# Kernel optimization log

Hardware: AMD Instinct MI355X
Metric: run time of the kernel (lower is better)

## Reference

```python
import jax, jax.numpy as jnp
import numpy as np

N_ROI = 116; G = 128; DEG = 32
N = G * N_ROI          # 14848 nodes
E = G * N_ROI * DEG    # 475136 edges
HID = 64; HEADS = 4; HC = HEADS * HID  # 256
EDIM = 5; EMB = 16; NG = 8; OUT = 2
NEG = 0.01      # nn.LeakyReLU default slope
NEG_ATT = 0.2   # GATv2 internal negative_slope
EPS = 1e-5


def leaky(x, s=NEG):
    return jnp.where(x >= 0, x, s * x)


def seg_softmax(logits, seg, n):
    # numerically stable softmax over edges grouped by target node
    m = jax.ops.segment_max(logits, seg, num_segments=n)
    m = jnp.where(jnp.isfinite(m), m, 0.0)
    ex = jnp.exp(logits - m[seg])
    s = jax.ops.segment_sum(ex, seg, num_segments=n)
    return ex / (s[seg] + 1e-16)


def _xav(k, shape):
    return jax.random.normal(k, shape, jnp.float32) * np.sqrt(2.0 / sum(shape)).astype(np.float32)


def setup_inputs() -> dict:
    key = jax.random.key(0)
    ks = jax.random.split(key, 40)
    x = jax.random.normal(ks[0], (N, N_ROI), jnp.float32)
    off = (jnp.arange(G, dtype=jnp.int32) * N_ROI)[:, None]
    src = (jax.random.randint(ks[1], (G, N_ROI * DEG), 0, N_ROI, jnp.int32) + off).reshape(-1)
    dst = (jax.random.randint(ks[2], (G, N_ROI * DEG), 0, N_ROI, jnp.int32) + off).reshape(-1)
    edge_index = jnp.stack([src, dst])  # [2, E], block-diagonal per graph
    edge_attr = jax.random.normal(ks[3], (E, EDIM), jnp.float32)
    grp = np.repeat(np.arange(NG, dtype=np.int32), [15] * 7 + [11])  # partition of 116 ROIs
    node_group = jnp.tile(jnp.asarray(grp), G)
    batch = jnp.repeat(jnp.arange(G, dtype=jnp.int32), N_ROI)
    p = {
        'group_emb': _xav(ks[4], (NG, EMB)),
        'W_embed': _xav(ks[5], (N_ROI + EMB, HID)), 'b_embed': jnp.zeros((HID,), jnp.float32),
        'We_enc': _xav(ks[6], (EDIM, HID)), 'be_enc': jnp.zeros((HID,), jnp.float32),
        'W1': _xav(ks[7], (HID, HID)), 'b1': jnp.zeros((HID,), jnp.float32),
        'W2': _xav(ks[8], (HID, HID)), 'b2': jnp.zeros((HID,), jnp.float32),
        'ln_g': jnp.ones((HID,), jnp.float32), 'ln_b': jnp.zeros((HID,), jnp.float32),
        'l0_Wl': _xav(ks[9], (HID, HC)), 'l0_Wr': _xav(ks[10], (HID, HC)),
        'l0_We': _xav(ks[11], (EDIM, HC)), 'l0_att': _xav(ks[12], (HEADS, HID)),
        'l0_b': jnp.zeros((HC,), jnp.float32),
        'l0_bn_g': jnp.ones((HC,), jnp.float32), 'l0_bn_b': jnp.zeros((HC,), jnp.float32),
        'l1_Wl': _xav(ks[13], (HC, HC)), 'l1_Wr': _xav(ks[14], (HC, HC)),
        'l1_We': _xav(ks[15], (EDIM, HC)), 'l1_att': _xav(ks[16], (HEADS, HID)),
        'l1_b': jnp.zeros((HC,), jnp.float32),
        'l1_bn_g': jnp.ones((HC,), jnp.float32), 'l1_bn_b': jnp.zeros((HC,), jnp.float32),
        'fc2_W': _xav(ks[17], (HC, OUT)), 'fc2_b': jnp.zeros((OUT,), jnp.float32),
    }
    return dict(x=x, edge_index=edge_index, edge_attr=edge_attr, batch=batch, node_group=node_group, **p)


def _gat_layer(h, src, dst, edge_attr, Wl, Wr, We, att, b, bn_g, bn_b):
    n = h.shape[0]
    xl = (h @ Wl).reshape(n, HEADS, HID)
    xr = (h @ Wr).reshape(n, HEADS, HID)
    e = (edge_attr @ We).reshape(-1, HEADS, HID)
    xls = xl[src]                                   # [E,H,C]
    z = leaky(xls + xr[dst] + e, NEG_ATT)
    logits = jnp.einsum('ehc,hc->eh', z, att)       # GATv2 attention scores
    alpha = seg_softmax(logits, dst, n)             # softmax over incoming edges per node
    out = jax.ops.segment_sum(xls * alpha[:, :, None], dst, num_segments=n)
    out = out.reshape(n, HC) + b
    mu = out.mean(0); var = ((out - mu) ** 2).mean(0)  # BatchNorm (batch stats)
    out = (out - mu) / jnp.sqrt(var + EPS) * bn_g + bn_b
    return leaky(out)


def reference(x, edge_index, edge_attr, batch, node_group, group_emb, W_embed, b_embed,
              We_enc, be_enc, W1, b1, W2, b2, ln_g, ln_b,
              l0_Wl, l0_Wr, l0_We, l0_att, l0_b, l0_bn_g, l0_bn_b,
              l1_Wl, l1_Wr, l1_We, l1_att, l1_b, l1_bn_g, l1_bn_b, fc2_W, fc2_b):
    src, dst = edge_index[0], edge_index[1]
    # BrainEncodeEmbed: group embedding concat + projection
    h = jnp.concatenate([x, group_emb[node_group]], axis=-1)   # [N, 132]
    h = leaky(h @ W_embed + b_embed)                            # [N, HID]
    eemb = leaky(edge_attr @ We_enc + be_enc)                   # [E, HID]
    # GINEConv: sum_j ReLU(x_j + e_ij), eps=0, then MLP
    msg = jax.nn.relu(h[src] + eemb)
    h = h + jax.ops.segment_sum(msg, dst, num_segments=N)
    h = leaky(h @ W1 + b1) @ W2 + b2
    h = leaky(h)
    mu = h.mean(-1, keepdims=True)
    v = ((h - mu) ** 2).mean(-1, keepdims=True)
    h = (h - mu) / jnp.sqrt(v + EPS) * ln_g + ln_b              # LayerNorm
    # stacked GATv2 blocks
    h = _gat_layer(h, src, dst, edge_attr, l0_Wl, l0_Wr, l0_We, l0_att, l0_b, l0_bn_g, l0_bn_b)
    h = _gat_layer(h, src, dst, edge_attr, l1_Wl, l1_Wr, l1_We, l1_att, l1_b, l1_bn_g, l1_bn_b)
    # global mean pool + classifier
    cnt = jax.ops.segment_sum(jnp.ones((h.shape[0],), h.dtype), batch, num_segments=G)
    pooled = jax.ops.segment_sum(h, batch, num_segments=G) / cnt[:, None]
    return pooled @ fc2_W + fc2_b
```

## Files before the change

### kernel.cpp

```cpp
#include <hip/hip_runtime.h>
#include <hip/hip_bf16.h>

#define NN     14848
#define NE     475136
#define NROI   116
#define NGRAPH 128
#define EPG    3712
#define HID    64
#define HC     256
#define NEG    0.01f
#define NEGA   0.2f
#define EPB    2304
#define XPAD   65

typedef __attribute__((ext_vector_type(8))) short short8;
typedef __attribute__((ext_vector_type(4))) float floatx4;

__device__ __forceinline__ float leaky(float x, float s) { return fmaxf(x, s * x); }

__device__ __forceinline__ short f2bf(float f) {
    unsigned u = __float_as_uint(f);
    unsigned r = (u + 0x7fffu + ((u >> 16) & 1u)) >> 16;
    return (short)r;
}

__global__ __launch_bounds__(256) void k_embed(
    const float* __restrict__ x, const int* __restrict__ ng,
    const float* __restrict__ gemb, const float* __restrict__ W,
    const float* __restrict__ b, float* __restrict__ h0)
{
    const int w = threadIdx.x >> 6, c = threadIdx.x & 63;
    const int n = blockIdx.x * 4 + w;
    __shared__ float in[4][132];
    for (int k = c; k < NROI; k += 64) in[w][k] = x[n * NROI + k];
    if (c < 16) in[w][NROI + c] = gemb[ng[n] * 16 + c];
    __syncthreads();
    float acc = b[c];
    #pragma unroll 4
    for (int k = 0; k < 132; k++) acc = fmaf(in[w][k], W[k * 64 + c], acc);
    h0[n * 64 + c] = leaky(acc, NEG);
}

__global__ __launch_bounds__(256) void k_csr(
    const int* __restrict__ src, const int* __restrict__ dst,
    const float* __restrict__ ea,
    int* __restrict__ row_start, int* __restrict__ row_cnt,
    int* __restrict__ ssd, float* __restrict__ ea_s,
    float* __restrict__ stats01)
{
    const int g = blockIdx.x, tid = threadIdx.x;
    if (g < 2) {
        for (int i = tid; i < 512; i += 256) stats01[g * 512 + i] = 0.f;
    }
    const int e0 = g * EPG, nb = g * NROI;
    __shared__ int cnt[NROI], start[NROI], cur[NROI];
    if (tid < NROI) cnt[tid] = 0;
    __syncthreads();
    for (int i = tid; i < EPG; i += 256) atomicAdd(&cnt[dst[e0 + i] - nb], 1);
    __syncthreads();
    if (tid == 0) {
        int s = 0;
        for (int r = 0; r < NROI; r++) { start[r] = s; s += cnt[r]; }
    }
    __syncthreads();
    if (tid < NROI) {
        row_start[nb + tid] = e0 + start[tid];
        row_cnt[nb + tid] = cnt[tid];
        cur[tid] = start[tid];
    }
    __syncthreads();
    for (int i = tid; i < EPG; i += 256) {
        const int e = e0 + i, dl = dst[e] - nb;
        const int pos = atomicAdd(&cur[dl], 1);
        const int gi = e0 + pos;
        ssd[gi] = (src[e] - nb) | (dl << 16);
        const float4 q = make_float4(ea[e * 5], ea[e * 5 + 1], ea[e * 5 + 2], ea[e * 5 + 3]);
        *(float4*)&ea_s[(size_t)gi * 8] = q;
        ea_s[(size_t)gi * 8 + 4] = ea[e * 5 + 4];
    }
}

__global__ __launch_bounds__(64) void k_prep_w(
    const float* __restrict__ Wl0, const float* __restrict__ Wr0,
    const float* __restrict__ Wl1, const float* __restrict__ Wr1,
    short* __restrict__ Wt0, short* __restrict__ Wt1)
{
    if (blockIdx.x < 512) {
        const int n = blockIdx.x;
        for (int k = threadIdx.x; k < 64; k += 64) {
            const float v = (n < 256) ? Wl0[k * 256 + n] : Wr0[k * 256 + (n - 256)];
            Wt0[(size_t)n * 64 + k] = f2bf(v);
        }
    } else {
        const int n = blockIdx.x - 512;
        for (int k = threadIdx.x; k < 256; k += 64) {
            const float v = (n < 256) ? Wl1[k * 256 + n] : Wr1[k * 256 + (n - 256)];
            Wt1[(size_t)n * 256 + k] = f2bf(v);
        }
    }
}

__global__ __launch_bounds__(256) void k_gine_mlp_ln(
    const float* __restrict__ h0, const int* __restrict__ row_start,
    const int* __restrict__ row_cnt, const int* __restrict__ ssd,
    const float* __restrict__ ea_s,
    const float* __restrict__ We, const float* __restrict__ be,
    const float* __restrict__ W1, const float* __restrict__ b1,
    const float* __restrict__ W2, const float* __restrict__ b2,
    const float* __restrict__ lg_, const float* __restrict__ lb_,
    short* __restrict__ hn)
{
    const int tid = threadIdx.x, w = tid >> 6, lane = tid & 63;
    const int row = blockIdx.x * 4 + w;
    const int nb = (row / NROI) * NROI;
    const int st = row_start[row], cnt = row_cnt[row];
    const float w0 = We[lane], w1 = We[64 + lane], w2 = We[128 + lane],
                w3 = We[192 + lane], w4 = We[256 + lane];
    const float bec = be[lane];
    float g0 = 0.f, g1 = 0.f;
    int j = 0;
    for (; j + 2 <= cnt; j += 2) {
        const int ia = st + j, ib = st + j + 1;
        const int sa = nb + (ssd[ia] & 0xffff), sb = nb + (ssd[ib] & 0xffff);
        const float4 qa = *(const float4*)&ea_s[(size_t)ia * 8];
        const float qa4 = ea_s[(size_t)ia * 8 + 4];
        const float4 qb = *(const float4*)&ea_s[(size_t)ib * 8];
        const float qb4 = ea_s[(size_t)ib * 8 + 4];
        float ea_ = bec, eb_ = bec;
        ea_ = fmaf(qa.x, w0, ea_); eb_ = fmaf(qb.x, w0, eb_);
        ea_ = fmaf(qa.y, w1, ea_); eb_ = fmaf(qb.y, w1, eb_);
        ea_ = fmaf(qa.z, w2, ea_); eb_ = fmaf(qb.z, w2, eb_);
        ea_ = fmaf(qa.w, w3, ea_); eb_ = fmaf(qb.w, w3, eb_);
        ea_ = fmaf(qa4, w4, ea_);  eb_ = fmaf(qb4, w4, eb_);
        g0 += fmaxf(h0[sa * 64 + lane] + leaky(ea_, NEG), 0.f);
        g1 += fmaxf(h0[sb * 64 + lane] + leaky(eb_, NEG), 0.f);
    }
    for (; j < cnt; j++) {
        const int idx = st + j;
        const int s = nb + (ssd[idx] & 0xffff);
        const float4 q = *(const float4*)&ea_s[(size_t)idx * 8];
        const float q4 = ea_s[(size_t)idx * 8 + 4];
        float em = bec;
        em = fmaf(q.x, w0, em); em = fmaf(q.y, w1, em); em = fmaf(q.z, w2, em);
        em = fmaf(q.w, w3, em); em = fmaf(q4, w4, em);
        g0 += fmaxf(h0[s * 64 + lane] + leaky(em, NEG), 0.f);
    }
    const float aggv = g0 + g1;
    __shared__ float v[4][64], t[4][64];
    v[w][lane] = h0[row * 64 + lane] + aggv;
    __syncthreads();
    float a = b1[lane];
    #pragma unroll 8
    for (int k = 0; k < 64; k++) a = fmaf(v[w][k], W1[k * 64 + lane], a);
    t[w][lane] = leaky(a, NEG);
    __syncthreads();
    float o = b2[lane];
    #pragma unroll 8
    for (int k = 0; k < 64; k++) o = fmaf(t[w][k], W2[k * 64 + lane], o);
    o = leaky(o, NEG);
    float s = o;
    #pragma unroll
    for (int off = 32; off; off >>= 1) s += __shfl_xor(s, off);
    const float mu = s * (1.f / 64.f);
    const float d = o - mu;
    float s2 = d * d;
    #pragma unroll
    for (int off = 32; off; off >>= 1) s2 += __shfl_xor(s2, off);
    hn[row * 64 + lane] = f2bf(d * rsqrtf(s2 * (1.f / 64.f) + 1e-5f) * lg_[lane] + lb_[lane]);
}

template <int D, bool BN>
__global__ __launch_bounds__(256) void k_gemm(
    const short* __restrict__ A, const float* __restrict__ Vin,
    const float* __restrict__ stats, const float* __restrict__ bn_g,
    const float* __restrict__ bn_b,
    const short* __restrict__ Wt,
    float* __restrict__ X, float* __restrict__ Y)
{
    const int m0 = blockIdx.x * 16;
    const int w = threadIdx.x >> 6, lane = threadIdx.x & 63;
    const int n0 = w * 128;
    const int r = lane & 15, q = lane >> 4;
    __shared__ float sc_s[256], sh_s[256];
    if constexpr (BN) {
        const int c = threadIdx.x;
        const float inv_n = 1.f / (float)NN;
        const float mu = stats[c] * inv_n;
        float var = stats[256 + c] * inv_n - mu * mu;
        var = fmaxf(var, 0.f);
        const float rsg = rsqrtf(var + 1e-5f) * bn_g[c];
        sc_s[c] = rsg;
        sh_s[c] = bn_b[c] - mu * rsg;
        __syncthreads();
    }
    floatx4 acc[8];
    #pragma unroll
    for (int t = 0; t < 8; t++) acc[t] = (floatx4){0.f, 0.f, 0.f, 0.f};
    const short* Arow = A + (size_t)(m0 + r) * D + q * 8;
    const float* Vrow = Vin + (size_t)(m0 + r) * D + q * 8;
    const short* Brow = Wt + (size_t)(n0 + r) * D + q * 8;
    #pragma unroll
    for (int k0 = 0; k0 < D; k0 += 32) {
        short8 a;
        if constexpr (BN) {
            const float4 v0 = *(const float4*)(Vrow + k0);
            const float4 v1 = *(const float4*)(Vrow + k0 + 4);
            const int cb = q * 8 + k0;
            a[0] = f2bf(leaky(fmaf(v0.x, sc_s[cb + 0], sh_s[cb + 0]), NEG));
            a[1] = f2bf(leaky(fmaf(v0.y, sc_s[cb + 1], sh_s[cb + 1]), NEG));
            a[2] = f2bf(leaky(fmaf(v0.z, sc_s[cb + 2], sh_s[cb + 2]), NEG));
            a[3] = f2bf(leaky(fmaf(v0.w, sc_s[cb + 3], sh_s[cb + 3]), NEG));
            a[4] = f2bf(leaky(fmaf(v1.x, sc_s[cb + 4], sh_s[cb + 4]), NEG));
            a[5] = f2bf(leaky(fmaf(v1.y, sc_s[cb + 5], sh_s[cb + 5]), NEG));
            a[6] = f2bf(leaky(fmaf(v1.z, sc_s[cb + 6], sh_s[cb + 6]), NEG));
            a[7] = f2bf(leaky(fmaf(v1.w, sc_s[cb + 7], sh_s[cb + 7]), NEG));
        } else {
            a = *(const short8*)(Arow + k0);
        }
        #pragma unroll
        for (int t = 0; t < 8; t++) {
            const short8 b = *(const short8*)(Brow + (size_t)t * 16 * D + k0);
            acc[t] = __builtin_amdgcn_mfma_f32_16x16x32_bf16(a, b, acc[t], 0, 0, 0);
        }
    }
    #pragma unroll
    for (int t = 0; t < 8; t++) {
        const int ncol = n0 + t * 16 + r;
        #pragma unroll
        for (int g2 = 0; g2 < 4; g2++) {
            const int row = m0 + q * 4 + g2;
            if (ncol < 256) X[(size_t)row * HC + ncol] = acc[t][g2];
            else            Y[(size_t)row * HC + (ncol - 256)] = acc[t][g2];
        }
    }
}

__global__ __launch_bounds__(256, 4) void k_gat(
    const int* __restrict__ row_start, const int* __restrict__ row_cnt,
    const int* __restrict__ ssd, const float* __restrict__ ea_s,
    const float* __restrict__ We, const float* __restrict__ att,
    const float* __restrict__ bias,
    const float* __restrict__ X, const float* __restrict__ Y,
    float* __restrict__ V, float* __restrict__ stats)
{
    const int g = blockIdx.x >> 3;
    const int h = (blockIdx.x >> 1) & 3;
    const int half = blockIdx.x & 1;
    const int tid = threadIdx.x, w = tid >> 6, lane = tid & 63;
    const int nb = g * NROI, e0 = g * EPG, hc = h * 64;
    const int r0 = half * 58, r1 = r0 + 58;
    const int es = row_start[nb + r0];
    const int ee = (r1 < NROI) ? row_start[nb + r1] : e0 + EPG;

    __shared__ float Xs[NROI * XPAD];
    __shared__ float lg[EPB];
    __shared__ float inv_s[58];

    for (int r = w; r < NROI; r += 4)
        Xs[r * XPAD + lane] = X[(size_t)(nb + r) * HC + hc + lane];
    __syncthreads();

    const int ne = ee - es;
    for (int i = tid; i < ne; i += 256) {
        const int e = es + i;
        const int sd = ssd[e];
        const int sl = sd & 0xffff, dl = sd >> 16;
        const float4 q = *(const float4*)&ea_s[(size_t)e * 8];
        const float q4 = ea_s[(size_t)e * 8 + 4];
        const float* yrow = &Y[(size_t)(nb + dl) * HC + hc];
        const int xb = sl * XPAD;
        float l0 = 0.f, l1 = 0.f;
        #pragma unroll 8
        for (int c = 0; c < 64; c += 2) {
            const float2 y2 = *(const float2*)(yrow + c);
            const float xs0 = Xs[xb + c], xs1 = Xs[xb + c + 1];
            float ep0 = q.x * We[0 * HC + hc + c];
            ep0 = fmaf(q.y, We[1 * HC + hc + c], ep0);
            ep0 = fmaf(q.z, We[2 * HC + hc + c], ep0);
            ep0 = fmaf(q.w, We[3 * HC + hc + c], ep0);
            ep0 = fmaf(q4, We[4 * HC + hc + c], ep0);
            float ep1 = q.x * We[0 * HC + hc + c + 1];
            ep1 = fmaf(q.y, We[1 * HC + hc + c + 1], ep1);
            ep1 = fmaf(q.z, We[2 * HC + hc + c + 1], ep1);
            ep1 = fmaf(q.w, We[3 * HC + hc + c + 1], ep1);
            ep1 = fmaf(q4, We[4 * HC + hc + c + 1], ep1);
            const float z0 = xs0 + y2.x + ep0;
            const float z1 = xs1 + y2.y + ep1;
            l0 = fmaf(att[hc + c], leaky(z0, NEGA), l0);
            l1 = fmaf(att[hc + c + 1], leaky(z1, NEGA), l1);
        }
        lg[i] = l0 + l1;
    }
    __syncthreads();

    for (int r = r0 + w; r < r1; r += 4) {
        const int stl = row_start[nb + r] - es;
        const int cnt = row_cnt[nb + r];
        float m = -INFINITY;
        for (int j = lane; j < cnt; j += 64) m = fmaxf(m, lg[stl + j]);
        #pragma unroll
        for (int off = 32; off; off >>= 1) m = fmaxf(m, __shfl_xor(m, off));
        float s = 0.f;
        for (int j = lane; j < cnt; j += 64) {
            const float e_ = __expf(lg[stl + j] - m);
            lg[stl + j] = e_;
            s += e_;
        }
        #pragma unroll
        for (int off = 32; off; off >>= 1) s += __shfl_xor(s, off);
        if (lane == 0) inv_s[r - r0] = 1.f / (s + 1e-16f);
    }
    __syncthreads();

    float ps = 0.f, ps2 = 0.f;
    const float bb = bias[hc + lane];
    for (int r = r0 + w; r < r1; r += 4) {
        const int st = row_start[nb + r];
        const int cnt = row_cnt[nb + r];
        const int stl = st - es;
        float a0 = 0.f, a1 = 0.f, a2 = 0.f, a3 = 0.f;
        int j = 0;
        for (; j + 4 <= cnt; j += 4) {
            const int s0 = ssd[st + j] & 0xffff, s1 = ssd[st + j + 1] & 0xffff,
                      s2 = ssd[st + j + 2] & 0xffff, s3 = ssd[st + j + 3] & 0xffff;
            a0 = fmaf(Xs[s0 * XPAD + lane], lg[stl + j], a0);
            a1 = fmaf(Xs[s1 * XPAD + lane], lg[stl + j + 1], a1);
            a2 = fmaf(Xs[s2 * XPAD + lane], lg[stl + j + 2], a2);
            a3 = fmaf(Xs[s3 * XPAD + lane], lg[stl + j + 3], a3);
        }
        for (; j < cnt; j++)
            a0 = fmaf(Xs[(ssd[st + j] & 0xffff) * XPAD + lane], lg[stl + j], a0);
        const float vv = ((a0 + a1) + (a2 + a3)) * inv_s[r - r0] + bb;
        V[(size_t)(nb + r) * HC + hc + lane] = vv;
        ps += vv;
        ps2 += vv * vv;
    }
    __syncthreads();
    lg[tid] = ps;
    lg[256 + tid] = ps2;
    __syncthreads();
    if (tid < 64) {
        float s1 = 0.f, s2 = 0.f;
        #pragma unroll
        for (int w2 = 0; w2 < 4; w2++) {
            s1 += lg[w2 * 64 + tid];
            s2 += lg[256 + w2 * 64 + tid];
        }
        atomicAdd(&stats[hc + tid], s1);
        atomicAdd(&stats[256 + hc + tid], s2);
    }
}

__global__ __launch_bounds__(256) void k_pool_fc(
    const float* __restrict__ V, const float* __restrict__ stats,
    const float* __restrict__ bg, const float* __restrict__ bb,
    const float* __restrict__ fW, const float* __restrict__ fb,
    float* __restrict__ out)
{
    const int g = blockIdx.x, c = threadIdx.x;
    const float inv_n = 1.f / (float)NN;
    const float mu = stats[c] * inv_n;
    float var = stats[256 + c] * inv_n - mu * mu;
    var = fmaxf(var, 0.f);
    const float rsg = rsqrtf(var + 1e-5f) * bg[c];
    const float bbc = bb[c];
    float s = 0.f;
    for (int r = 0; r < NROI; r++) {
        const float vv = (V[(size_t)(g * NROI + r) * HC + c] - mu) * rsg + bbc;
        s += leaky(vv, NEG);
    }
    s *= (1.f / (float)NROI);
    __shared__ float red[256];
    for (int o = 0; o < 2; o++) {
        red[c] = s * fW[c * 2 + o];
        __syncthreads();
        for (int off = 128; off; off >>= 1) {
            if (c < off) red[c] += red[c + off];
            __syncthreads();
        }
        if (c == 0) out[g * 2 + o] = red[0] + fb[o];
        __syncthreads();
    }
}

extern "C" void kernel_launch(void* const* d_in, const int* in_sizes, int n_in,
                              void* d_out, int out_size, void* d_ws, size_t ws_size,
                              hipStream_t stream) {
    const float* x         = (const float*)d_in[0];
    const int*   edge_idx  = (const int*)d_in[1];
    const float* edge_attr = (const float*)d_in[2];
    const int*   node_grp  = (const int*)d_in[4];
    const float* group_emb = (const float*)d_in[5];
    const float* W_embed   = (const float*)d_in[6];
    const float* b_embed   = (const float*)d_in[7];
    const float* We_enc    = (const float*)d_in[8];
    const float* be_enc    = (const float*)d_in[9];
    const float* W1        = (const float*)d_in[10];
    const float* b1        = (const float*)d_in[11];
    const float* W2        = (const float*)d_in[12];
    const float* b2        = (const float*)d_in[13];
    const float* ln_g      = (const float*)d_in[14];
    const float* ln_b      = (const float*)d_in[15];
    const float* l0_Wl     = (const float*)d_in[16];
    const float* l0_Wr     = (const float*)d_in[17];
    const float* l0_We     = (const float*)d_in[18];
    const float* l0_att    = (const float*)d_in[19];
    const float* l0_b      = (const float*)d_in[20];
    const float* l0_bn_g   = (const float*)d_in[21];
    const float* l0_bn_b   = (const float*)d_in[22];
    const float* l1_Wl     = (const float*)d_in[23];
    const float* l1_Wr     = (const float*)d_in[24];
    const float* l1_We     = (const float*)d_in[25];
    const float* l1_att    = (const float*)d_in[26];
    const float* l1_b      = (const float*)d_in[27];
    const float* l1_bn_g   = (const float*)d_in[28];
    const float* l1_bn_b   = (const float*)d_in[29];
    const float* fc2_W     = (const float*)d_in[30];
    const float* fc2_b     = (const float*)d_in[31];

    const int* src = edge_idx;
    const int* dst = edge_idx + NE;

    float* ws     = (float*)d_ws;
    float* h0     = ws;
    float* X      = h0 + (size_t)64 * NN;
    float* Y      = X + (size_t)HC * NN;
    float* V      = Y + (size_t)HC * NN;
    float* stats0 = V + (size_t)HC * NN;
    float* stats1 = stats0 + 512;
    float* ea_s   = stats1 + 512;
    int* row_start = (int*)(ea_s + (size_t)8 * NE);
    int* row_cnt   = row_start + NN;
    int* ssd       = row_cnt + NN;
    short* hn_b    = (short*)(ssd + NE);
    short* Wt0     = hn_b + (size_t)64 * NN;
    short* Wt1     = Wt0 + 512 * 64;

    float* out = (float*)d_out;

    k_embed<<<NN / 4, 256, 0, stream>>>(x, node_grp, group_emb, W_embed, b_embed, h0);
    k_csr<<<NGRAPH, 256, 0, stream>>>(src, dst, edge_attr, row_start, row_cnt, ssd, ea_s, stats0);
    k_prep_w<<<1024, 64, 0, stream>>>(l0_Wl, l0_Wr, l1_Wl, l1_Wr, Wt0, Wt1);
    k_gine_mlp_ln<<<NN / 4, 256, 0, stream>>>(h0, row_start, row_cnt, ssd, ea_s,
                                              We_enc, be_enc, W1, b1, W2, b2, ln_g, ln_b, hn_b);

    k_gemm<64, false><<<NN / 16, 256, 0, stream>>>(hn_b, nullptr, nullptr, nullptr, nullptr,
                                                   Wt0, X, Y);
    k_gat<<<NGRAPH * 8, 256, 0, stream>>>(row_start, row_cnt, ssd, ea_s,
                                          l0_We, l0_att, l0_b, X, Y, V, stats0);

    k_gemm<256, true><<<NN / 16, 256, 0, stream>>>(nullptr, V, stats0, l0_bn_g, l0_bn_b,
                                                   Wt1, X, Y);
    k_gat<<<NGRAPH * 8, 256, 0, stream>>>(row_start, row_cnt, ssd, ea_s,
                                          l1_We, l1_att, l1_b, X, Y, V, stats1);

    k_pool_fc<<<NGRAPH, 256, 0, stream>>>(V, stats1, l1_bn_g, l1_bn_b, fc2_W, fc2_b, out);
}
```

Measured before the change: 451.9 us.

## Merge front-end kernels, unroll GINE gather by four, pack GAT logits into float2

Merges the embed, CSR build and weight-prep kernels into one launch that dispatches on block index, removing two kernel launches and their serialization. Unrolls the GINE neighbor-gather loop from two edges to four so more independent loads are in flight. Rewrites the GAT logit inner loop with float2 vector types so the compiler can emit packed FP32 math and wider loads. The weight-prep blocks now run 256 threads where only 64 or 256 do work, which wastes lanes in those blocks.

Measured after the change: 430.7 us. 4.7% less time.

```diff
diff --git a/kernel.cpp b/kernel.cpp
--- a/kernel.cpp
+++ b/kernel.cpp
@@ -15,6 +15,7 @@
 
 typedef __attribute__((ext_vector_type(8))) short short8;
 typedef __attribute__((ext_vector_type(4))) float floatx4;
+typedef __attribute__((ext_vector_type(2))) float floatx2;
 
 __device__ __forceinline__ float leaky(float x, float s) { return fmaxf(x, s * x); }
 
@@ -24,78 +25,76 @@
     return (short)r;
 }
 
-__global__ __launch_bounds__(256) void k_embed(
+__global__ __launch_bounds__(256) void k_front(
     const float* __restrict__ x, const int* __restrict__ ng,
     const float* __restrict__ gemb, const float* __restrict__ W,
-    const float* __restrict__ b, float* __restrict__ h0)
-{
-    const int w = threadIdx.x >> 6, c = threadIdx.x & 63;
-    const int n = blockIdx.x * 4 + w;
-    __shared__ float in[4][132];
-    for (int k = c; k < NROI; k += 64) in[w][k] = x[n * NROI + k];
-    if (c < 16) in[w][NROI + c] = gemb[ng[n] * 16 + c];
-    __syncthreads();
-    float acc = b[c];
-    #pragma unroll 4
-    for (int k = 0; k < 132; k++) acc = fmaf(in[w][k], W[k * 64 + c], acc);
-    h0[n * 64 + c] = leaky(acc, NEG);
-}
-
-__global__ __launch_bounds__(256) void k_csr(
+    const float* __restrict__ b, float* __restrict__ h0,
     const int* __restrict__ src, const int* __restrict__ dst,
     const float* __restrict__ ea,
     int* __restrict__ row_start, int* __restrict__ row_cnt,
     int* __restrict__ ssd, float* __restrict__ ea_s,
-    float* __restrict__ stats01)
-{
-    const int g = blockIdx.x, tid = threadIdx.x;
-    if (g < 2) {
-        for (int i = tid; i < 512; i += 256) stats01[g * 512 + i] = 0.f;
-    }
-    const int e0 = g * EPG, nb = g * NROI;
-    __shared__ int cnt[NROI], start[NROI], cur[NROI];
-    if (tid < NROI) cnt[tid] = 0;
-    __syncthreads();
-    for (int i = tid; i < EPG; i += 256) atomicAdd(&cnt[dst[e0 + i] - nb], 1);
-    __syncthreads();
-    if (tid == 0) {
-        int s = 0;
-        for (int r = 0; r < NROI; r++) { start[r] = s; s += cnt[r]; }
-    }
-    __syncthreads();
-    if (tid < NROI) {
-        row_start[nb + tid] = e0 + start[tid];
-        row_cnt[nb + tid] = cnt[tid];
-        cur[tid] = start[tid];
-    }
-    __syncthreads();
-    for (int i = tid; i < EPG; i += 256) {
-        const int e = e0 + i, dl = dst[e] - nb;
-        const int pos = atomicAdd(&cur[dl], 1);
-        const int gi = e0 + pos;
-        ssd[gi] = (src[e] - nb) | (dl << 16);
-        const float4 q = make_float4(ea[e * 5], ea[e * 5 + 1], ea[e * 5 + 2], ea[e * 5 + 3]);
-        *(float4*)&ea_s[(size_t)gi * 8] = q;
-        ea_s[(size_t)gi * 8 + 4] = ea[e * 5 + 4];
-    }
-}
-
-__global__ __launch_bounds__(64) void k_prep_w(
+    float* __restrict__ stats01,
     const float* __restrict__ Wl0, const float* __restrict__ Wr0,
     const float* __restrict__ Wl1, const float* __restrict__ Wr1,
     short* __restrict__ Wt0, short* __restrict__ Wt1)
 {
-    if (blockIdx.x < 512) {
-        const int n = blockIdx.x;
-        for (int k = threadIdx.x; k < 64; k += 64) {
-            const float v = (n < 256) ? Wl0[k * 256 + n] : Wr0[k * 256 + (n - 256)];
-            Wt0[(size_t)n * 64 + k] = f2bf(v);
+    const int tid = threadIdx.x;
+    if (blockIdx.x < NN / 4) {
+        const int w = tid >> 6, c = tid & 63;
+        const int n = blockIdx.x * 4 + w;
+        __shared__ float in[4][132];
+        for (int k = c; k < NROI; k += 64) in[w][k] = x[n * NROI + k];
+        if (c < 16) in[w][NROI + c] = gemb[ng[n] * 16 + c];
+        __syncthreads();
+        float acc = b[c];
+        #pragma unroll 4
+        for (int k = 0; k < 132; k++) acc = fmaf(in[w][k], W[k * 64 + c], acc);
+        h0[n * 64 + c] = leaky(acc, NEG);
+    } else if (blockIdx.x < NN / 4 + NGRAPH) {
+        const int g = blockIdx.x - NN / 4;
+        if (g < 2) {
+            for (int i = tid; i < 512; i += 256) stats01[g * 512 + i] = 0.f;
+        }
+        const int e0 = g * EPG, nb = g * NROI;
+        __shared__ int cnt[NROI], start[NROI], cur[NROI];
+        if (tid < NROI) cnt[tid] = 0;
+        __syncthreads();
+        for (int i = tid; i < EPG; i += 256) atomicAdd(&cnt[dst[e0 + i] - nb], 1);
+        __syncthreads();
+        if (tid == 0) {
+            int s = 0;
+            for (int r = 0; r < NROI; r++) { start[r] = s; s += cnt[r]; }
+        }
+        __syncthreads();
+        if (tid < NROI) {
+            row_start[nb + tid] = e0 + start[tid];
+            row_cnt[nb + tid] = cnt[tid];
+            cur[tid] = start[tid];
+        }
+        __syncthreads();
+        for (int i = tid; i < EPG; i += 256) {
+            const int e = e0 + i, dl = dst[e] - nb;
+            const int pos = atomicAdd(&cur[dl], 1);
+            const int gi = e0 + pos;
+            ssd[gi] = (src[e] - nb) | (dl << 16);
+            const float4 q = make_float4(ea[e * 5], ea[e * 5 + 1], ea[e * 5 + 2], ea[e * 5 + 3]);
+            *(float4*)&ea_s[(size_t)gi * 8] = q;
+            ea_s[(size_t)gi * 8 + 4] = ea[e * 5 + 4];
         }
     } else {
-        const int n = blockIdx.x - 512;
-        for (int k = threadIdx.x; k < 256; k += 64) {
-            const float v = (n < 256) ? Wl1[k * 256 + n] : Wr1[k * 256 + (n - 256)];
-            Wt1[(size_t)n * 256 + k] = f2bf(v);
+        const int bb = blockIdx.x - (NN / 4 + NGRAPH);
+        if (bb < 512) {
+            const int n = bb;
+            for (int k = tid; k < 64; k += 256) {
+                const float v = (n < 256) ? Wl0[k * 256 + n] : Wr0[k * 256 + (n - 256)];
+                Wt0[(size_t)n * 64 + k] = f2bf(v);
+            }
+        } else {
+            const int n = bb - 512;
+            for (int k = tid; k < 256; k += 256) {
+                const float v = (n < 256) ? Wl1[k * 256 + n] : Wr1[k * 256 + (n - 256)];
+                Wt1[(size_t)n * 256 + k] = f2bf(v);
+            }
         }
     }
 }
@@ -117,23 +116,37 @@
     const float w0 = We[lane], w1 = We[64 + lane], w2 = We[128 + lane],
                 w3 = We[192 + lane], w4 = We[256 + lane];
     const float bec = be[lane];
-    float g0 = 0.f, g1 = 0.f;
+    float g0 = 0.f, g1 = 0.f, g2 = 0.f, g3 = 0.f;
     int j = 0;
-    for (; j + 2 <= cnt; j += 2) {
-        const int ia = st + j, ib = st + j + 1;
-        const int sa = nb + (ssd[ia] & 0xffff), sb = nb + (ssd[ib] & 0xffff);
-        const float4 qa = *(const float4*)&ea_s[(size_t)ia * 8];
-        const float qa4 = ea_s[(size_t)ia * 8 + 4];
-        const float4 qb = *(const float4*)&ea_s[(size_t)ib * 8];
-        const float qb4 = ea_s[(size_t)ib * 8 + 4];
-        float ea_ = bec, eb_ = bec;
-        ea_ = fmaf(qa.x, w0, ea_); eb_ = fmaf(qb.x, w0, eb_);
-        ea_ = fmaf(qa.y, w1, ea_); eb_ = fmaf(qb.y, w1, eb_);
-        ea_ = fmaf(qa.z, w2, ea_); eb_ = fmaf(qb.z, w2, eb_);
-        ea_ = fmaf(qa.w, w3, ea_); eb_ = fmaf(qb.w, w3, eb_);
-        ea_ = fmaf(qa4, w4, ea_);  eb_ = fmaf(qb4, w4, eb_);
-        g0 += fmaxf(h0[sa * 64 + lane] + leaky(ea_, NEG), 0.f);
-        g1 += fmaxf(h0[sb * 64 + lane] + leaky(eb_, NEG), 0.f);
+    for (; j + 4 <= cnt; j += 4) {
+        const int i0 = st + j, i1 = st + j + 1, i2 = st + j + 2, i3 = st + j + 3;
+        const int s0 = nb + (ssd[i0] & 0xffff), s1 = nb + (ssd[i1] & 0xffff),
+                  s2 = nb + (ssd[i2] & 0xffff), s3 = nb + (ssd[i3] & 0xffff);
+        const float h_0 = h0[s0 * 64 + lane], h_1 = h0[s1 * 64 + lane],
+                    h_2 = h0[s2 * 64 + lane], h_3 = h0[s3 * 64 + lane];
+        const float4 qa = *(const float4*)&ea_s[(size_t)i0 * 8];
+        const float qa4 = ea_s[(size_t)i0 * 8 + 4];
+        const float4 qb = *(const float4*)&ea_s[(size_t)i1 * 8];
+        const float qb4 = ea_s[(size_t)i1 * 8 + 4];
+        const float4 qc = *(const float4*)&ea_s[(size_t)i2 * 8];
+        const float qc4 = ea_s[(size_t)i2 * 8 + 4];
+        const float4 qd = *(const float4*)&ea_s[(size_t)i3 * 8];
+        const float qd4 = ea_s[(size_t)i3 * 8 + 4];
+        float e0_ = bec, e1_ = bec, e2_ = bec, e3_ = bec;
+        e0_ = fmaf(qa.x, w0, e0_); e1_ = fmaf(qb.x, w0, e1_);
+        e2_ = fmaf(qc.x, w0, e2_); e3_ = fmaf(qd.x, w0, e3_);
+        e0_ = fmaf(qa.y, w1, e0_); e1_ = fmaf(qb.y, w1, e1_);
+        e2_ = fmaf(qc.y, w1, e2_); e3_ = fmaf(qd.y, w1, e3_);
+        e0_ = fmaf(qa.z, w2, e0_); e1_ = fmaf(qb.z, w2, e1_);
+        e2_ = fmaf(qc.z, w2, e2_); e3_ = fmaf(qd.z, w2, e3_);
+        e0_ = fmaf(qa.w, w3, e0_); e1_ = fmaf(qb.w, w3, e1_);
+        e2_ = fmaf(qc.w, w3, e2_); e3_ = fmaf(qd.w, w3, e3_);
+        e0_ = fmaf(qa4, w4, e0_);  e1_ = fmaf(qb4, w4, e1_);
+        e2_ = fmaf(qc4, w4, e2_);  e3_ = fmaf(qd4, w4, e3_);
+        g0 += fmaxf(h_0 + leaky(e0_, NEG), 0.f);
+        g1 += fmaxf(h_1 + leaky(e1_, NEG), 0.f);
+        g2 += fmaxf(h_2 + leaky(e2_, NEG), 0.f);
+        g3 += fmaxf(h_3 + leaky(e3_, NEG), 0.f);
     }
     for (; j < cnt; j++) {
         const int idx = st + j;
@@ -145,7 +158,7 @@
         em = fmaf(q.w, w3, em); em = fmaf(q4, w4, em);
         g0 += fmaxf(h0[s * 64 + lane] + leaky(em, NEG), 0.f);
     }
-    const float aggv = g0 + g1;
+    const float aggv = (g0 + g1) + (g2 + g3);
     __shared__ float v[4][64], t[4][64];
     v[w][lane] = h0[row * 64 + lane] + aggv;
     __syncthreads();
@@ -267,29 +280,32 @@
         const int sl = sd & 0xffff, dl = sd >> 16;
         const float4 q = *(const float4*)&ea_s[(size_t)e * 8];
         const float q4 = ea_s[(size_t)e * 8 + 4];
+        const floatx2 qx = {q.x, q.x}, qy = {q.y, q.y}, qz = {q.z, q.z},
+                      qw = {q.w, q.w}, qv = {q4, q4};
         const float* yrow = &Y[(size_t)(nb + dl) * HC + hc];
         const int xb = sl * XPAD;
-        float l0 = 0.f, l1 = 0.f;
+        floatx2 lacc = {0.f, 0.f};
         #pragma unroll 8
         for (int c = 0; c < 64; c += 2) {
-            const float2 y2 = *(const float2*)(yrow + c);
-            const float xs0 = Xs[xb + c], xs1 = Xs[xb + c + 1];
-            float ep0 = q.x * We[0 * HC + hc + c];
-            ep0 = fmaf(q.y, We[1 * HC + hc + c], ep0);
-            ep0 = fmaf(q.z, We[2 * HC + hc + c], ep0);
-            ep0 = fmaf(q.w, We[3 * HC + hc + c], ep0);
-            ep0 = fmaf(q4, We[4 * HC + hc + c], ep0);
-            float ep1 = q.x * We[0 * HC + hc + c + 1];
-            ep1 = fmaf(q.y, We[1 * HC + hc + c + 1], ep1);
-            ep1 = fmaf(q.z, We[2 * HC + hc + c + 1], ep1);
-            ep1 = fmaf(q.w, We[3 * HC + hc + c + 1], ep1);
-            ep1 = fmaf(q4, We[4 * HC + hc + c + 1], ep1);
-            const float z0 = xs0 + y2.x + ep0;
-            const float z1 = xs1 + y2.y + ep1;
-            l0 = fmaf(att[hc + c], leaky(z0, NEGA), l0);
-            l1 = fmaf(att[hc + c + 1], leaky(z1, NEGA), l1);
-        }
-        lg[i] = l0 + l1;
+            const floatx2 y2 = *(const floatx2*)(yrow + c);
+            const floatx2 xs2 = {Xs[xb + c], Xs[xb + c + 1]};
+            const floatx2 w0 = *(const floatx2*)(We + 0 * HC + hc + c);
+            const floatx2 w1 = *(const floatx2*)(We + 1 * HC + hc + c);
+            const floatx2 w2 = *(const floatx2*)(We + 2 * HC + hc + c);
+            const floatx2 w3 = *(const floatx2*)(We + 3 * HC + hc + c);
+            const floatx2 w4 = *(const floatx2*)(We + 4 * HC + hc + c);
+            floatx2 ep = qx * w0;
+            ep += qy * w1;
+            ep += qz * w2;
+            ep += qw * w3;
+            ep += qv * w4;
+            const floatx2 z = xs2 + y2 + ep;
+            const floatx2 zs = z * (floatx2){NEGA, NEGA};
+            const floatx2 lk = {fmaxf(z.x, zs.x), fmaxf(z.y, zs.y)};
+            const floatx2 a2 = *(const floatx2*)(att + hc + c);
+            lacc += a2 * lk;
+        }
+        lg[i] = lacc.x + lacc.y;
     }
     __syncthreads();
 
@@ -438,9 +454,10 @@
 
     float* out = (float*)d_out;
 
-    k_embed<<<NN / 4, 256, 0, stream>>>(x, node_grp, group_emb, W_embed, b_embed, h0);
-    k_csr<<<NGRAPH, 256, 0, stream>>>(src, dst, edge_attr, row_start, row_cnt, ssd, ea_s, stats0);
-    k_prep_w<<<1024, 64, 0, stream>>>(l0_Wl, l0_Wr, l1_Wl, l1_Wr, Wt0, Wt1);
+    k_front<<<NN / 4 + NGRAPH + 1024, 256, 0, stream>>>(
+        x, node_grp, group_emb, W_embed, b_embed, h0,
+        src, dst, edge_attr, row_start, row_cnt, ssd, ea_s, stats0,
+        l0_Wl, l0_Wr, l1_Wl, l1_Wr, Wt0, Wt1);
     k_gine_mlp_ln<<<NN / 4, 256, 0, stream>>>(h0, row_start, row_cnt, ssd, ea_s,
                                               We_enc, be_enc, W1, b1, W2, b2, ln_g, ln_b, hn_b);
 
```
